# Performance work log

Measured on AMD Instinct MI355X. Metric: run time of the kernel, lower is better.

Reference implementation:

```python
import jax, jax.numpy as jnp
import numpy as np

EPS = 1e-5
N_HEADS = 8
NEG = -1e32


def _pos_emb(S, D):
    # CosinePositionalEmbedding: sin/cos fully overwrite the random init for even D
    pos = jnp.arange(S, dtype=jnp.float32)[:, None]
    div = jnp.exp(jnp.arange(0, D, 2, dtype=jnp.float32) * (-np.log(10000.0) / D))
    pe = jnp.zeros((S, D), dtype=jnp.float32)
    pe = pe.at[:, 0::2].set(jnp.sin(pos * div))
    pe = pe.at[:, 1::2].set(jnp.cos(pos * div))
    return pe


def _ln(x, g, b):
    mu = jnp.mean(x, axis=-1, keepdims=True)
    var = jnp.mean((x - mu) ** 2, axis=-1, keepdims=True)
    return (x - mu) / jnp.sqrt(var + EPS) * g + b


def setup_inputs() -> dict:
    key = jax.random.key(0)
    B, S, D, FF, L = 32, 512, 512, 2048, 4
    ks = jax.random.split(key, 8)
    w = 0.02
    return {
        "q_embed_data": jax.random.normal(ks[0], (B, S, D), jnp.float32),
        "qa_embed_data": jax.random.normal(ks[1], (B, S, D), jnp.float32),
        "boost_focus": jax.random.uniform(ks[2], (1,), jnp.float32),
        "Wk": w * jax.random.normal(ks[3], (L, D, D), jnp.float32),
        "bk": jnp.zeros((L, D), jnp.float32),
        "Wv": w * jax.random.normal(ks[4], (L, D, D), jnp.float32),
        "bv": jnp.zeros((L, D), jnp.float32),
        "Wo": w * jax.random.normal(ks[5], (L, D, D), jnp.float32),
        "bo": jnp.zeros((L, D), jnp.float32),
        "ln1_g": jnp.ones((L, D), jnp.float32),
        "ln1_b": jnp.zeros((L, D), jnp.float32),
        "W1": w * jax.random.normal(ks[6], (L, D, FF), jnp.float32),
        "b1": jnp.zeros((L, FF), jnp.float32),
        "W2": w * jax.random.normal(ks[7], (L, FF, D), jnp.float32),
        "b2": jnp.zeros((L, D), jnp.float32),
        "ln2_g": jnp.ones((L, D), jnp.float32),
        "ln2_b": jnp.zeros((L, D), jnp.float32),
    }


def reference(q_embed_data, qa_embed_data, boost_focus, Wk, bk, Wv, bv, Wo, bo,
              ln1_g, ln1_b, W1, b1, W2, b2, ln2_g, ln2_b):
    B, S, D = q_embed_data.shape
    L = Wk.shape[0]
    H = N_HEADS
    dk = D // H
    bf = boost_focus[0]
    pe = _pos_emb(S, D)
    x = q_embed_data + pe[None]          # query/key stream
    y = qa_embed_data + pe[None]         # value stream (fixed across blocks)
    # mask=0: triu(k=0)==0 -> only strictly past positions (j < i) allowed
    allowed = jnp.tril(jnp.ones((S, S), bool), k=-1)
    scale = 1.0 / np.sqrt(dk)
    for l in range(L):
        # kq_same=True: q and k both use k_linear on x -> identical projections
        qk = (x @ Wk[l] + bk[l]).reshape(B, S, H, dk).transpose(0, 2, 1, 3)
        v = (y @ Wv[l] + bv[l]).reshape(B, S, H, dk).transpose(0, 2, 1, 3)
        scores = jnp.einsum('bhid,bhjd->bhij', qk, qk) * scale * (1.0 + bf)
        scores = jnp.where(allowed, scores, NEG)
        probs = jax.nn.softmax(scores, axis=-1)
        probs = probs.at[:, :, 0, :].set(0.0)  # zero_pad: first query row zeroed
        attn = jnp.einsum('bhij,bhjd->bhid', probs, v)
        attn = attn.transpose(0, 2, 1, 3).reshape(B, S, D) @ Wo[l] + bo[l]
        x = _ln(x + attn, ln1_g[l], ln1_b[l])
        ff = jax.nn.relu(x @ W1[l] + b1[l]) @ W2[l] + b2[l]
        x = _ln(x + ff, ln2_g[l], ln2_b[l])
    return x
```

## Files before the change

### kernel.cpp

```cpp
#include <hip/hip_runtime.h>
#include <hip/hip_bf16.h>

typedef __bf16 bf16_t;
typedef __bf16 bf16x4 __attribute__((ext_vector_type(4)));
typedef __bf16 bf16x8 __attribute__((ext_vector_type(8)));
typedef float f32x4 __attribute__((ext_vector_type(4)));

union FragU { bf16x8 v; bf16x4 h[2]; };
union F4U { float4 v; float f[4]; };

constexpr int BB = 32, SS = 512, DD = 512, FFD = 2048, LL = 4, HH = 8;

__device__ __forceinline__ int permk(int k) {
  int g = (k >> 2) & 7;
  int pos = (g < 4) ? (g << 1) : (((g - 4) << 1) | 1);
  return (k & ~31) | (pos << 2) | (k & 3);
}

__device__ __forceinline__ void gload_lds16(const bf16_t* g, bf16_t* l) {
  __builtin_amdgcn_global_load_lds(
      (const __attribute__((address_space(1))) void*)g,
      (__attribute__((address_space(3))) void*)l, 16, 0, 0);
}

__global__ void pe_kernel(float* __restrict__ pe) {
  int idx = blockIdx.x * blockDim.x + threadIdx.x;
  if (idx >= SS * DD / 2) return;
  int p = idx % (DD / 2);
  int s = idx / (DD / 2);
  float div = expf((float)(2 * p) * (-9.210340371976184f / (float)DD));
  float a = (float)s * div;
  pe[s * DD + 2 * p]     = sinf(a);
  pe[s * DD + 2 * p + 1] = cosf(a);
}

__global__ __launch_bounds__(256) void tcast_kernel(const float* __restrict__ src,
                                                    bf16_t* __restrict__ dst,
                                                    int K, int N) {
  __shared__ float tile[32][33];
  size_t mat = (size_t)blockIdx.z * (size_t)K * (size_t)N;
  int k0 = blockIdx.y * 32, n0 = blockIdx.x * 32;
  int t = threadIdx.x;
  int r = t >> 3, c4 = (t & 7) * 4;
  const float4 v = *reinterpret_cast<const float4*>(&src[mat + (size_t)(k0 + r) * N + n0 + c4]);
  tile[r][c4 + 0] = v.x; tile[r][c4 + 1] = v.y; tile[r][c4 + 2] = v.z; tile[r][c4 + 3] = v.w;
  __syncthreads();
  bf16x4 o;
  o[0] = (bf16_t)tile[c4 + 0][r];
  o[1] = (bf16_t)tile[c4 + 1][r];
  o[2] = (bf16_t)tile[c4 + 2][r];
  o[3] = (bf16_t)tile[c4 + 3][r];
  *reinterpret_cast<bf16x4*>(&dst[mat + permk((n0 + r) * K + k0 + c4)]) = o;
}

__global__ void addpe_kernel(const float* __restrict__ q, const float* __restrict__ qa,
                             const float* __restrict__ pe,
                             float* __restrict__ x, bf16_t* __restrict__ xb,
                             bf16_t* __restrict__ yb) {
  int i = blockIdx.x * blockDim.x + threadIdx.x;
  int pei = i & (SS * DD / 4 - 1);
  float4 pv = reinterpret_cast<const float4*>(pe)[pei];
  float4 qv = reinterpret_cast<const float4*>(q)[i];
  float4 av = reinterpret_cast<const float4*>(qa)[i];
  float4 xv = make_float4(qv.x + pv.x, qv.y + pv.y, qv.z + pv.z, qv.w + pv.w);
  float4 yv = make_float4(av.x + pv.x, av.y + pv.y, av.z + pv.z, av.w + pv.w);
  reinterpret_cast<float4*>(x)[i] = xv;
  bf16x4 xo, yo;
  xo[0] = (bf16_t)xv.x; xo[1] = (bf16_t)xv.y; xo[2] = (bf16_t)xv.z; xo[3] = (bf16_t)xv.w;
  yo[0] = (bf16_t)yv.x; yo[1] = (bf16_t)yv.y; yo[2] = (bf16_t)yv.z; yo[3] = (bf16_t)yv.w;
  int kp = permk(4 * i);
  *reinterpret_cast<bf16x4*>(&xb[kp]) = xo;
  *reinterpret_cast<bf16x4*>(&yb[kp]) = yo;
}

template<bool OUT_BF16, bool RELU>
__global__ __launch_bounds__(256, 2) void gemm_kernel(const bf16_t* __restrict__ A,
                                                      const bf16_t* __restrict__ Bt,
                                                      const float* __restrict__ bias,
                                                      void* __restrict__ Cout,
                                                      int M, int N, int K, int nnt) {
  __shared__ bf16_t a_s[2][128 * 64];
  __shared__ bf16_t b_s[2][128 * 64];
  const int t = threadIdx.x;
  const int nwg = gridDim.x;
  const int bid = blockIdx.x;
  const int wg = (bid & 7) * (nwg >> 3) + (bid >> 3);
  const int m0 = (wg / nnt) * 128, n0 = (wg % nnt) * 128;
  const int l = t & 63, w = t >> 6, g = l >> 4, ln = l & 15;
  const int wm = (w >> 1) * 64, wn = (w & 1) * 64;
  const int tr = t >> 3;
  const int bsrc = ((t & 7) ^ (tr & 7)) * 8;
  const bf16_t* Asrc = A + (size_t)(m0 + tr) * K + bsrc;
  const bf16_t* Bsrc = Bt + (size_t)(n0 + tr) * K + bsrc;
  const size_t rstr = (size_t)32 * K;
  const int x0 = (g ^ (ln & 7)) * 8;
  const int x1 = ((4 + g) ^ (ln & 7)) * 8;
  f32x4 acc[4][4] = {};
  const int NT = K >> 6;
#pragma unroll
  for (int i = 0; i < 4; i++) gload_lds16(Asrc + i * rstr, &a_s[0][(i * 256 + t) * 8]);
#pragma unroll
  for (int i = 0; i < 4; i++) gload_lds16(Bsrc + i * rstr, &b_s[0][(i * 256 + t) * 8]);
  asm volatile("s_waitcnt vmcnt(0)" ::: "memory");
  __syncthreads();
  for (int tt = 0; tt < NT; tt++) {
    const int cur = tt & 1;
    if (tt + 1 < NT) {
      const int k1 = (tt + 1) << 6;
#pragma unroll
      for (int i = 0; i < 4; i++) gload_lds16(Asrc + k1 + i * rstr, &a_s[cur ^ 1][(i * 256 + t) * 8]);
#pragma unroll
      for (int i = 0; i < 4; i++) gload_lds16(Bsrc + k1 + i * rstr, &b_s[cur ^ 1][(i * 256 + t) * 8]);
    }
#pragma unroll
    for (int kc = 0; kc < 2; kc++) {
      const int xo = kc ? x1 : x0;
      FragU fa[4], fb[4];
#pragma unroll
      for (int mi = 0; mi < 4; mi++)
        fa[mi].v = *reinterpret_cast<const bf16x8*>(&a_s[cur][(wm + mi * 16 + ln) * 64 + xo]);
#pragma unroll
      for (int ni = 0; ni < 4; ni++)
        fb[ni].v = *reinterpret_cast<const bf16x8*>(&b_s[cur][(wn + ni * 16 + ln) * 64 + xo]);
      __builtin_amdgcn_s_setprio(1);
#pragma unroll
      for (int mi = 0; mi < 4; mi++)
#pragma unroll
        for (int ni = 0; ni < 4; ni++)
          acc[mi][ni] = __builtin_amdgcn_mfma_f32_16x16x32_bf16(fa[mi].v, fb[ni].v, acc[mi][ni], 0, 0, 0);
      __builtin_amdgcn_s_setprio(0);
    }
    asm volatile("s_waitcnt vmcnt(0)" ::: "memory");
    __syncthreads();
  }
#pragma unroll
  for (int ni = 0; ni < 4; ni++) {
    const int col = n0 + wn + ni * 16 + ln;
    const float bv = bias[col];
    const int colp = OUT_BF16 ? permk(col) : col;
#pragma unroll
    for (int mi = 0; mi < 4; mi++)
#pragma unroll
      for (int r = 0; r < 4; r++) {
        int row = m0 + wm + mi * 16 + g * 4 + r;
        float o = acc[mi][ni][r] + bv;
        if (RELU) o = fmaxf(o, 0.f);
        if (OUT_BF16)
          reinterpret_cast<bf16_t*>(Cout)[(size_t)row * N + colp] = (bf16_t)o;
        else
          reinterpret_cast<float*>(Cout)[(size_t)row * N + col] = o;
      }
  }
}

__global__ __launch_bounds__(256) void ln_kernel(const float* __restrict__ xin,
                                                 const float* __restrict__ addv,
                                                 const float* __restrict__ gamma,
                                                 const float* __restrict__ beta,
                                                 float* __restrict__ xout,
                                                 bf16_t* __restrict__ xbout) {
  int row = blockIdx.x * 4 + (threadIdx.x >> 6);
  int l = threadIdx.x & 63;
  const float* px = xin + (size_t)row * DD;
  const float* pa = addv + (size_t)row * DD;
  float vals[8];
  float s = 0.f;
#pragma unroll
  for (int i = 0; i < 2; i++) {
    float4 a = reinterpret_cast<const float4*>(px)[l * 2 + i];
    float4 b = reinterpret_cast<const float4*>(pa)[l * 2 + i];
    vals[i * 4 + 0] = a.x + b.x;
    vals[i * 4 + 1] = a.y + b.y;
    vals[i * 4 + 2] = a.z + b.z;
    vals[i * 4 + 3] = a.w + b.w;
  }
#pragma unroll
  for (int j = 0; j < 8; j++) s += vals[j];
#pragma unroll
  for (int off = 1; off < 64; off <<= 1) s += __shfl_xor(s, off, 64);
  float mean = s * (1.f / DD);
  float sq = 0.f;
#pragma unroll
  for (int j = 0; j < 8; j++) { float d = vals[j] - mean; sq += d * d; }
#pragma unroll
  for (int off = 1; off < 64; off <<= 1) sq += __shfl_xor(sq, off, 64);
  float rstd = rsqrtf(sq * (1.f / DD) + 1e-5f);
#pragma unroll
  for (int i = 0; i < 2; i++) {
    F4U o; bf16x4 ob;
#pragma unroll
    for (int j = 0; j < 4; j++) {
      int colj = l * 8 + i * 4 + j;
      float v = (vals[i * 4 + j] - mean) * rstd * gamma[colj] + beta[colj];
      o.f[j] = v;
      ob[j] = (bf16_t)v;
    }
    reinterpret_cast<float4*>(xout + (size_t)row * DD)[l * 2 + i] = o.v;
    *reinterpret_cast<bf16x4*>(&xbout[(size_t)row * DD + permk(l * 8 + i * 4)]) = ob;
  }
}

__global__ __launch_bounds__(256) void vtrans_kernel(const bf16_t* __restrict__ vbuf,
                                                     bf16_t* __restrict__ vtg) {
  __shared__ bf16_t t_s[64][72];
  const int jt = blockIdx.x, h = blockIdx.y, b = blockIdx.z;
  const int t = threadIdx.x;
#pragma unroll
  for (int i = 0; i < 2; i++) {
    int c = t + i * 256;
    int s = c >> 3, bb = c & 7;
    FragU vr;
    vr.v = *reinterpret_cast<const bf16x8*>(
        &vbuf[(size_t)(b * SS + jt * 64 + s) * DD + h * 64 + bb * 8]);
    int cc = (bb >> 2) * 32, p = (bb & 3) * 4;
    *reinterpret_cast<bf16x4*>(&t_s[s][cc + p]) = vr.h[0];
    *reinterpret_cast<bf16x4*>(&t_s[s][cc + 16 + p]) = vr.h[1];
  }
  __syncthreads();
#pragma unroll
  for (int i = 0; i < 2; i++) {
    int c = t + i * 256;
    int d = c >> 3, blkx = c & 7;
    int blk = blkx ^ (d & 7);
    int js = blk >> 2, g = blk & 3;
    FragU o;
#pragma unroll
    for (int e = 0; e < 4; e++) o.v[e] = t_s[js * 32 + g * 4 + e][d];
#pragma unroll
    for (int e = 0; e < 4; e++) o.v[e + 4] = t_s[js * 32 + 16 + g * 4 + e][d];
    *reinterpret_cast<bf16x8*>(
        &vtg[((size_t)((b * HH + h) * 64 + d)) * SS + jt * 64 + blkx * 8]) = o.v;
  }
}

__global__ __launch_bounds__(256) void attn_kernel(const bf16_t* __restrict__ qk,
                                                   const bf16_t* __restrict__ vtg,
                                                   bf16_t* __restrict__ outp,
                                                   const float* __restrict__ bfp) {
  __shared__ bf16_t k_s[64 * 64];
  __shared__ bf16_t v_t[64 * 64];
  const int bx = blockIdx.x, h = blockIdx.y, b = blockIdx.z;
  const int t = threadIdx.x, l = t & 63, w = t >> 6, g = l >> 4, ln = l & 15;
  const float sc = 0.125f * (1.f + bfp[0]);
  const size_t base = ((size_t)b * SS) * DD + h * 64;
  const bf16_t* vbase = vtg + ((size_t)((b * HH + h) * 64)) * SS;
  const int NQT = SS / 64;

  for (int pass = 0; pass < 2; pass++) {
    const int qt = pass ? (NQT - 1 - bx) : bx;
    const int i0 = qt * 64;
    FragU qB[2];
    {
      const bf16_t* qp = qk + base + (size_t)(i0 + w * 16 + ln) * DD;
      qB[0].v = *reinterpret_cast<const bf16x8*>(&qp[g * 8]);
      qB[1].v = *reinterpret_cast<const bf16x8*>(&qp[32 + g * 8]);
    }
    float m = -1e30f, lrow = 0.f;
    f32x4 acc[4] = {};
    const int iql = w * 16 + ln;

    for (int kt = 0; kt <= qt; kt++) {
      const int j0 = kt * 64;
      __syncthreads();
      {
        int c1 = t + 256;
        int jr0 = t >> 3, bb0 = t & 7;
        int jr1 = c1 >> 3, bb1 = c1 & 7;
        gload_lds16(qk + base + (size_t)(j0 + jr0) * DD + ((bb0 ^ (jr0 & 7)) * 8), &k_s[t * 8]);
        gload_lds16(qk + base + (size_t)(j0 + jr1) * DD + ((bb1 ^ (jr1 & 7)) * 8), &k_s[c1 * 8]);
        gload_lds16(vbase + (size_t)jr0 * SS + j0 + bb0 * 8, &v_t[t * 8]);
        gload_lds16(vbase + (size_t)jr1 * SS + j0 + bb1 * 8, &v_t[c1 * 8]);
      }
      asm volatile("s_waitcnt vmcnt(0)" ::: "memory");
      __syncthreads();
      f32x4 sfr[4] = {};
#pragma unroll
      for (int ks = 0; ks < 2; ks++)
#pragma unroll
        for (int nj = 0; nj < 4; nj++) {
          int jc = nj * 16 + ln;
          FragU ka;
          ka.v = *reinterpret_cast<const bf16x8*>(&k_s[jc * 64 + (((ks * 4 + g) ^ (jc & 7)) * 8)]);
          sfr[nj] = __builtin_amdgcn_mfma_f32_16x16x32_bf16(ka.v, qB[ks].v, sfr[nj], 0, 0, 0);
        }
      if (kt == qt) {
#pragma unroll
        for (int nj = 0; nj < 4; nj++)
#pragma unroll
          for (int r = 0; r < 4; r++)
            if (nj * 16 + g * 4 + r >= iql) sfr[nj][r] = -1e30f;
      }
      float pm = -1e30f;
#pragma unroll
      for (int nj = 0; nj < 4; nj++)
#pragma unroll
        for (int r = 0; r < 4; r++) pm = fmaxf(pm, sfr[nj][r]);
      pm = fmaxf(pm, __shfl_xor(pm, 16, 64));
      pm = fmaxf(pm, __shfl_xor(pm, 32, 64));
      float mnew = fmaxf(m, pm);
      float fac = __expf(sc * (m - mnew));
      m = mnew;
      float ps = 0.f;
#pragma unroll
      for (int nj = 0; nj < 4; nj++)
#pragma unroll
        for (int r = 0; r < 4; r++) {
          float p = __expf(sc * (sfr[nj][r] - m));
          sfr[nj][r] = p;
          ps += p;
        }
      ps += __shfl_xor(ps, 16, 64);
      ps += __shfl_xor(ps, 32, 64);
      lrow = lrow * fac + ps;
      float facr[4];
#pragma unroll
      for (int r = 0; r < 4; r++) facr[r] = __shfl(fac, g * 4 + r, 64);
#pragma unroll
      for (int nd = 0; nd < 4; nd++)
#pragma unroll
        for (int r = 0; r < 4; r++) acc[nd][r] *= facr[r];
      FragU pa[2];
#pragma unroll
      for (int js = 0; js < 2; js++)
#pragma unroll
        for (int kk = 0; kk < 4; kk++) {
          pa[js].v[kk]     = (bf16_t)sfr[js * 2][kk];
          pa[js].v[kk + 4] = (bf16_t)sfr[js * 2 + 1][kk];
        }
#pragma unroll
      for (int js = 0; js < 2; js++)
#pragma unroll
        for (int nd = 0; nd < 4; nd++) {
          int d = nd * 16 + ln;
          FragU vb;
          vb.v = *reinterpret_cast<const bf16x8*>(&v_t[d * 64 + (((js * 4 + g) ^ (d & 7)) * 8)]);
          acc[nd] = __builtin_amdgcn_mfma_f32_16x16x32_bf16(pa[js].v, vb.v, acc[nd], 0, 0, 0);
        }
    }
    float lr[4];
#pragma unroll
    for (int r = 0; r < 4; r++) lr[r] = __shfl(lrow, g * 4 + r, 64);
    const int orow0 = i0 + w * 16 + g * 4;
#pragma unroll
    for (int nd = 0; nd < 4; nd++) {
      const int colp = permk(nd * 16 + ln);
#pragma unroll
      for (int r = 0; r < 4; r++) {
        int grow = orow0 + r;
        float o = (grow > 0 && lr[r] > 0.f) ? acc[nd][r] / lr[r] : 0.f;
        outp[base + (size_t)grow * DD + colp] = (bf16_t)o;
      }
    }
  }
}

extern "C" void kernel_launch(void* const* d_in, const int* in_sizes, int n_in,
                              void* d_out, int out_size, void* d_ws, size_t ws_size,
                              hipStream_t stream) {
  const float* q_emb  = (const float*)d_in[0];
  const float* qa_emb = (const float*)d_in[1];
  const float* bfp    = (const float*)d_in[2];
  const float* Wk  = (const float*)d_in[3];
  const float* bk  = (const float*)d_in[4];
  const float* Wv  = (const float*)d_in[5];
  const float* bv  = (const float*)d_in[6];
  const float* Wo  = (const float*)d_in[7];
  const float* bo  = (const float*)d_in[8];
  const float* g1  = (const float*)d_in[9];
  const float* be1 = (const float*)d_in[10];
  const float* W1  = (const float*)d_in[11];
  const float* b1  = (const float*)d_in[12];
  const float* W2  = (const float*)d_in[13];
  const float* b2  = (const float*)d_in[14];
  const float* g2  = (const float*)d_in[15];
  const float* be2 = (const float*)d_in[16];
  float* out = (float*)d_out;
  (void)in_sizes; (void)n_in; (void)out_size; (void)ws_size;

  char* wsp = (char*)d_ws;
  size_t off = 0;
  auto alloc = [&](size_t bytes) -> void* {
    void* p = wsp + off;
    off += (bytes + 255) & ~(size_t)255;
    return p;
  };
  const size_t BSD = (size_t)BB * SS * DD;
  float*  pe   = (float*) alloc((size_t)SS * DD * 4);
  float*  x    = (float*) alloc(BSD * 4);
  float*  tmp  = (float*) alloc(BSD * 4);
  bf16_t* xb   = (bf16_t*)alloc(BSD * 2);
  bf16_t* yb   = (bf16_t*)alloc(BSD * 2);
  bf16_t* qkb  = (bf16_t*)alloc(BSD * 2);
  bf16_t* vbuf = (bf16_t*)alloc(BSD * 2);
  bf16_t* vtg  = (bf16_t*)alloc(BSD * 2);
  bf16_t* atb  = (bf16_t*)alloc(BSD * 2);
  bf16_t* h1   = (bf16_t*)alloc((size_t)BB * SS * FFD * 2);
  bf16_t* Wkb  = (bf16_t*)alloc((size_t)LL * DD * DD * 2);
  bf16_t* Wvb  = (bf16_t*)alloc((size_t)LL * DD * DD * 2);
  bf16_t* Wob  = (bf16_t*)alloc((size_t)LL * DD * DD * 2);
  bf16_t* W1b  = (bf16_t*)alloc((size_t)LL * DD * FFD * 2);
  bf16_t* W2b  = (bf16_t*)alloc((size_t)LL * FFD * DD * 2);

  pe_kernel<<<(SS * DD / 2 + 255) / 256, 256, 0, stream>>>(pe);
  tcast_kernel<<<dim3(DD / 32, DD / 32, LL), 256, 0, stream>>>(Wk, Wkb, DD, DD);
  tcast_kernel<<<dim3(DD / 32, DD / 32, LL), 256, 0, stream>>>(Wv, Wvb, DD, DD);
  tcast_kernel<<<dim3(DD / 32, DD / 32, LL), 256, 0, stream>>>(Wo, Wob, DD, DD);
  tcast_kernel<<<dim3(FFD / 32, DD / 32, LL), 256, 0, stream>>>(W1, W1b, DD, FFD);
  tcast_kernel<<<dim3(DD / 32, FFD / 32, LL), 256, 0, stream>>>(W2, W2b, FFD, DD);
  addpe_kernel<<<(int)(BSD / 4 / 256), 256, 0, stream>>>(q_emb, qa_emb, pe, x, xb, yb);

  const int M = BB * SS;
  const int nD = (M / 128) * (DD / 128);
  const int nF = (M / 128) * (FFD / 128);
  dim3 gA(SS / 128, HH, BB);
  dim3 gV(SS / 64, HH, BB);
  for (int layer = 0; layer < LL; layer++) {
    const bf16_t* Wkl = Wkb + (size_t)layer * DD * DD;
    const bf16_t* Wvl = Wvb + (size_t)layer * DD * DD;
    const bf16_t* Wol = Wob + (size_t)layer * DD * DD;
    const bf16_t* W1l = W1b + (size_t)layer * DD * FFD;
    const bf16_t* W2l = W2b + (size_t)layer * FFD * DD;
    gemm_kernel<true, false><<<nD, 256, 0, stream>>>(xb, Wkl, bk + layer * DD, qkb, M, DD, DD, DD / 128);
    gemm_kernel<true, false><<<nD, 256, 0, stream>>>(yb, Wvl, bv + layer * DD, vbuf, M, DD, DD, DD / 128);
    vtrans_kernel<<<gV, 256, 0, stream>>>(vbuf, vtg);
    attn_kernel<<<gA, 256, 0, stream>>>(qkb, vtg, atb, bfp);
    gemm_kernel<false, false><<<nD, 256, 0, stream>>>(atb, Wol, bo + layer * DD, tmp, M, DD, DD, DD / 128);
    ln_kernel<<<M / 4, 256, 0, stream>>>(x, tmp, g1 + layer * DD, be1 + layer * DD, x, xb);
    gemm_kernel<true, true><<<nF, 256, 0, stream>>>(xb, W1l, b1 + layer * FFD, h1, M, FFD, DD, FFD / 128);
    gemm_kernel<false, false><<<nD, 256, 0, stream>>>(h1, W2l, b2 + layer * DD, tmp, M, DD, FFD, DD / 128);
    float* xo = (layer == LL - 1) ? out : x;
    ln_kernel<<<M / 4, 256, 0, stream>>>(x, tmp, g2 + layer * DD, be2 + layer * DD, xo, xb);
  }
}
```

Before: 888.0 us.

## Replace GEMM with 8-wave 256-row tile kernel using ping-pong MFMA scheduling

Swaps the 128x128 tile, 4-wave GEMM for an 8-wave (512-thread) kernel with 256-row tiles, using 128 or 256 columns depending on the layer. Global-to-LDS loads now run two stages ahead, and LDS fragment reads are interleaved with MFMA clusters between barriers, in the style of the HipKittens 8-wave schedule. The larger tiles are meant to improve data reuse and keep the matrix units busy. In exchange, register pressure and barrier count go up, and the K/V/O GEMMs get fewer workgroups, which can hurt occupancy.

```diff
diff --git a/kernel.cpp b/kernel.cpp
--- a/kernel.cpp
+++ b/kernel.cpp
@@ -22,6 +22,12 @@
       (const __attribute__((address_space(1))) void*)g,
       (__attribute__((address_space(3))) void*)l, 16, 0, 0);
 }
+
+template<int N> __device__ __forceinline__ void vmwait() {
+  asm volatile("s_waitcnt vmcnt(%0)" :: "n"(N) : "memory");
+}
+
+#define MFMA_ACC(d, a, b) d = __builtin_amdgcn_mfma_f32_16x16x32_bf16((a).v, (b).v, d, 0, 0, 0)
 
 __global__ void pe_kernel(float* __restrict__ pe) {
   int idx = blockIdx.x * blockDim.x + threadIdx.x;
@@ -73,77 +79,177 @@
   *reinterpret_cast<bf16x4*>(&yb[kp]) = yo;
 }
 
-template<bool OUT_BF16, bool RELU>
-__global__ __launch_bounds__(256, 2) void gemm_kernel(const bf16_t* __restrict__ A,
-                                                      const bf16_t* __restrict__ Bt,
-                                                      const float* __restrict__ bias,
-                                                      void* __restrict__ Cout,
-                                                      int M, int N, int K, int nnt) {
-  __shared__ bf16_t a_s[2][128 * 64];
-  __shared__ bf16_t b_s[2][128 * 64];
+template<int BN, bool OUT_BF16, bool RELU>
+__global__ __launch_bounds__(512, 2) void gemm8_kernel(const bf16_t* __restrict__ A,
+                                                       const bf16_t* __restrict__ Bt,
+                                                       const float* __restrict__ bias,
+                                                       void* __restrict__ Cout,
+                                                       int N, int K, int nnt) {
+  constexpr int BM = 256, BK = 64;
+  constexpr int WN = BN / 4;
+  constexpr int NF = WN / 16;
+  constexpr int AL = 4, BL = BN / 64;
+  constexpr int LOADS = AL + BL;
+  __shared__ bf16_t a_s[2][BM * BK];
+  __shared__ bf16_t b_s[2][BN * BK];
   const int t = threadIdx.x;
-  const int nwg = gridDim.x;
-  const int bid = blockIdx.x;
+  const int bid = blockIdx.x, nwg = gridDim.x;
   const int wg = (bid & 7) * (nwg >> 3) + (bid >> 3);
-  const int m0 = (wg / nnt) * 128, n0 = (wg % nnt) * 128;
-  const int l = t & 63, w = t >> 6, g = l >> 4, ln = l & 15;
-  const int wm = (w >> 1) * 64, wn = (w & 1) * 64;
-  const int tr = t >> 3;
-  const int bsrc = ((t & 7) ^ (tr & 7)) * 8;
-  const bf16_t* Asrc = A + (size_t)(m0 + tr) * K + bsrc;
-  const bf16_t* Bsrc = Bt + (size_t)(n0 + tr) * K + bsrc;
-  const size_t rstr = (size_t)32 * K;
-  const int x0 = (g ^ (ln & 7)) * 8;
-  const int x1 = ((4 + g) ^ (ln & 7)) * 8;
-  f32x4 acc[4][4] = {};
+  const int m0 = (wg / nnt) * BM, n0 = (wg % nnt) * BN;
+  const int l = t & 63, w = t >> 6, g = l >> 4, ln = l & 15, lnx = l & 7;
+  const int wr = w >> 2, wc = w & 3;
+  const int tr8 = t >> 3;
+  const int bsrc = ((t & 7) ^ (tr8 & 7)) * 8;
+  const bf16_t* Asrc = A + (size_t)(m0 + tr8) * K + bsrc;
+  const bf16_t* Bsrc = Bt + (size_t)(n0 + tr8) * K + bsrc;
+  const size_t rstr = (size_t)64 * K;
+
+  auto STAGE = [&](int p, int kt) {
+    const int k0 = kt << 6;
+#pragma unroll
+    for (int i = 0; i < AL; i++) gload_lds16(Asrc + k0 + i * rstr, &a_s[p][(i * 512 + t) * 8]);
+#pragma unroll
+    for (int i = 0; i < BL; i++) gload_lds16(Bsrc + k0 + i * rstr, &b_s[p][(i * 512 + t) * 8]);
+  };
+  auto rdA = [&](int p, int mh, int mi, int kc) -> bf16x8 {
+    return *reinterpret_cast<const bf16x8*>(
+        &a_s[p][(wr * 128 + mh * 64 + mi * 16 + ln) * 64 + ((kc * 4 + g) ^ lnx) * 8]);
+  };
+  auto rdB = [&](int p, int nf, int kc) -> bf16x8 {
+    return *reinterpret_cast<const bf16x8*>(
+        &b_s[p][(wc * WN + nf * 16 + ln) * 64 + ((kc * 4 + g) ^ lnx) * 8]);
+  };
+
+  f32x4 acc[8][NF] = {};
   const int NT = K >> 6;
-#pragma unroll
-  for (int i = 0; i < 4; i++) gload_lds16(Asrc + i * rstr, &a_s[0][(i * 256 + t) * 8]);
-#pragma unroll
-  for (int i = 0; i < 4; i++) gload_lds16(Bsrc + i * rstr, &b_s[0][(i * 256 + t) * 8]);
-  asm volatile("s_waitcnt vmcnt(0)" ::: "memory");
+  STAGE(0, 0);
+  STAGE(1, 1);
+  vmwait<LOADS>();
   __syncthreads();
-  for (int tt = 0; tt < NT; tt++) {
-    const int cur = tt & 1;
-    if (tt + 1 < NT) {
-      const int k1 = (tt + 1) << 6;
-#pragma unroll
-      for (int i = 0; i < 4; i++) gload_lds16(Asrc + k1 + i * rstr, &a_s[cur ^ 1][(i * 256 + t) * 8]);
-#pragma unroll
-      for (int i = 0; i < 4; i++) gload_lds16(Bsrc + k1 + i * rstr, &b_s[cur ^ 1][(i * 256 + t) * 8]);
+
+  for (int T = 0; T < NT; T++) {
+    const int p = T & 1;
+    if constexpr (BN == 256) {
+      FragU fa[8], fbA[4], fbB[4];
+#pragma unroll
+      for (int kc = 0; kc < 2; kc++) {
+#pragma unroll
+        for (int mi = 0; mi < 4; mi++) fa[kc * 4 + mi].v = rdA(p, 0, mi, kc);
+#pragma unroll
+        for (int ni = 0; ni < 2; ni++) fbA[kc * 2 + ni].v = rdB(p, ni, kc);
+      }
+      __syncthreads();
+      __builtin_amdgcn_s_setprio(1);
+#pragma unroll
+      for (int kc = 0; kc < 2; kc++)
+#pragma unroll
+        for (int mi = 0; mi < 4; mi++)
+#pragma unroll
+          for (int ni = 0; ni < 2; ni++)
+            MFMA_ACC(acc[mi][ni], fa[kc * 4 + mi], fbA[kc * 2 + ni]);
+      __builtin_amdgcn_s_setprio(0);
+      __syncthreads();
+#pragma unroll
+      for (int kc = 0; kc < 2; kc++)
+#pragma unroll
+        for (int ni = 0; ni < 2; ni++) fbB[kc * 2 + ni].v = rdB(p, 2 + ni, kc);
+      __syncthreads();
+      __builtin_amdgcn_s_setprio(1);
+#pragma unroll
+      for (int kc = 0; kc < 2; kc++)
+#pragma unroll
+        for (int mi = 0; mi < 4; mi++)
+#pragma unroll
+          for (int ni = 0; ni < 2; ni++)
+            MFMA_ACC(acc[mi][2 + ni], fa[kc * 4 + mi], fbB[kc * 2 + ni]);
+      __builtin_amdgcn_s_setprio(0);
+      __syncthreads();
+#pragma unroll
+      for (int kc = 0; kc < 2; kc++)
+#pragma unroll
+        for (int mi = 0; mi < 4; mi++) fa[kc * 4 + mi].v = rdA(p, 1, mi, kc);
+      __syncthreads();
+      __builtin_amdgcn_s_setprio(1);
+#pragma unroll
+      for (int kc = 0; kc < 2; kc++)
+#pragma unroll
+        for (int mi = 0; mi < 4; mi++)
+#pragma unroll
+          for (int ni = 0; ni < 2; ni++)
+            MFMA_ACC(acc[4 + mi][2 + ni], fa[kc * 4 + mi], fbB[kc * 2 + ni]);
+      __builtin_amdgcn_s_setprio(0);
+      __syncthreads();
+      if (T + 2 < NT) STAGE(p, T + 2);
+      __syncthreads();
+      __builtin_amdgcn_s_setprio(1);
+#pragma unroll
+      for (int kc = 0; kc < 2; kc++)
+#pragma unroll
+        for (int mi = 0; mi < 4; mi++)
+#pragma unroll
+          for (int ni = 0; ni < 2; ni++)
+            MFMA_ACC(acc[4 + mi][ni], fa[kc * 4 + mi], fbA[kc * 2 + ni]);
+      __builtin_amdgcn_s_setprio(0);
+      if (T + 1 < NT) { if (T + 2 < NT) vmwait<LOADS>(); else vmwait<0>(); }
+      __syncthreads();
+    } else {
+      FragU fa0[8], fa1[8], fb[4];
+#pragma unroll
+      for (int kc = 0; kc < 2; kc++) {
+#pragma unroll
+        for (int mi = 0; mi < 4; mi++) fa0[kc * 4 + mi].v = rdA(p, 0, mi, kc);
+#pragma unroll
+        for (int ni = 0; ni < 2; ni++) fb[kc * 2 + ni].v = rdB(p, ni, kc);
+      }
+      __syncthreads();
+      __builtin_amdgcn_s_setprio(1);
+#pragma unroll
+      for (int mi = 0; mi < 4; mi++)
+#pragma unroll
+        for (int ni = 0; ni < 2; ni++)
+          MFMA_ACC(acc[mi][ni], fa0[mi], fb[ni]);
+      __builtin_amdgcn_s_setprio(0);
+      __syncthreads();
+#pragma unroll
+      for (int kc = 0; kc < 2; kc++)
+#pragma unroll
+        for (int mi = 0; mi < 4; mi++) fa1[kc * 4 + mi].v = rdA(p, 1, mi, kc);
+      __syncthreads();
+      __builtin_amdgcn_s_setprio(1);
+#pragma unroll
+      for (int mi = 0; mi < 4; mi++)
+#pragma unroll
+        for (int ni = 0; ni < 2; ni++)
+          MFMA_ACC(acc[mi][ni], fa0[4 + mi], fb[2 + ni]);
+      __builtin_amdgcn_s_setprio(0);
+      __syncthreads();
+      if (T + 2 < NT) STAGE(p, T + 2);
+      __syncthreads();
+      __builtin_amdgcn_s_setprio(1);
+#pragma unroll
+      for (int kc = 0; kc < 2; kc++)
+#pragma unroll
+        for (int mi = 0; mi < 4; mi++)
+#pragma unroll
+          for (int ni = 0; ni < 2; ni++)
+            MFMA_ACC(acc[4 + mi][ni], fa1[kc * 4 + mi], fb[kc * 2 + ni]);
+      __builtin_amdgcn_s_setprio(0);
+      if (T + 1 < NT) { if (T + 2 < NT) vmwait<LOADS>(); else vmwait<0>(); }
+      __syncthreads();
     }
-#pragma unroll
-    for (int kc = 0; kc < 2; kc++) {
-      const int xo = kc ? x1 : x0;
-      FragU fa[4], fb[4];
-#pragma unroll
-      for (int mi = 0; mi < 4; mi++)
-        fa[mi].v = *reinterpret_cast<const bf16x8*>(&a_s[cur][(wm + mi * 16 + ln) * 64 + xo]);
-#pragma unroll
-      for (int ni = 0; ni < 4; ni++)
-        fb[ni].v = *reinterpret_cast<const bf16x8*>(&b_s[cur][(wn + ni * 16 + ln) * 64 + xo]);
-      __builtin_amdgcn_s_setprio(1);
-#pragma unroll
-      for (int mi = 0; mi < 4; mi++)
-#pragma unroll
-        for (int ni = 0; ni < 4; ni++)
-          acc[mi][ni] = __builtin_amdgcn_mfma_f32_16x16x32_bf16(fa[mi].v, fb[ni].v, acc[mi][ni], 0, 0, 0);
-      __builtin_amdgcn_s_setprio(0);
-    }
-    asm volatile("s_waitcnt vmcnt(0)" ::: "memory");
-    __syncthreads();
-  }
-#pragma unroll
-  for (int ni = 0; ni < 4; ni++) {
-    const int col = n0 + wn + ni * 16 + ln;
+  }
+
+#pragma unroll
+  for (int nf = 0; nf < NF; nf++) {
+    const int col = n0 + wc * WN + nf * 16 + ln;
     const float bv = bias[col];
     const int colp = OUT_BF16 ? permk(col) : col;
 #pragma unroll
-    for (int mi = 0; mi < 4; mi++)
+    for (int mf = 0; mf < 8; mf++)
 #pragma unroll
       for (int r = 0; r < 4; r++) {
-        int row = m0 + wm + mi * 16 + g * 4 + r;
-        float o = acc[mi][ni][r] + bv;
+        int row = m0 + wr * 128 + mf * 16 + g * 4 + r;
+        float o = acc[mf][nf][r] + bv;
         if (RELU) o = fmaxf(o, 0.f);
         if (OUT_BF16)
           reinterpret_cast<bf16_t*>(Cout)[(size_t)row * N + colp] = (bf16_t)o;
@@ -410,8 +516,8 @@
   addpe_kernel<<<(int)(BSD / 4 / 256), 256, 0, stream>>>(q_emb, qa_emb, pe, x, xb, yb);
 
   const int M = BB * SS;
-  const int nD = (M / 128) * (DD / 128);
-  const int nF = (M / 128) * (FFD / 128);
+  const int nD8 = (M / 256) * (DD / 128);
+  const int nF8 = (M / 256) * (FFD / 256);
   dim3 gA(SS / 128, HH, BB);
   dim3 gV(SS / 64, HH, BB);
   for (int layer = 0; layer < LL; layer++) {
@@ -420,14 +526,14 @@
     const bf16_t* Wol = Wob + (size_t)layer * DD * DD;
     const bf16_t* W1l = W1b + (size_t)layer * DD * FFD;
     const bf16_t* W2l = W2b + (size_t)layer * FFD * DD;
-    gemm_kernel<true, false><<<nD, 256, 0, stream>>>(xb, Wkl, bk + layer * DD, qkb, M, DD, DD, DD / 128);
-    gemm_kernel<true, false><<<nD, 256, 0, stream>>>(yb, Wvl, bv + layer * DD, vbuf, M, DD, DD, DD / 128);
+    gemm8_kernel<128, true, false><<<nD8, 512, 0, stream>>>(xb, Wkl, bk + layer * DD, qkb, DD, DD, DD / 128);
+    gemm8_kernel<128, true, false><<<nD8, 512, 0, stream>>>(yb, Wvl, bv + layer * DD, vbuf, DD, DD, DD / 128);
     vtrans_kernel<<<gV, 256, 0, stream>>>(vbuf, vtg);
     attn_kernel<<<gA, 256, 0, stream>>>(qkb, vtg, atb, bfp);
-    gemm_kernel<false, false><<<nD, 256, 0, stream>>>(atb, Wol, bo + layer * DD, tmp, M, DD, DD, DD / 128);
+    gemm8_kernel<128, false, false><<<nD8, 512, 0, stream>>>(atb, Wol, bo + layer * DD, tmp, DD, DD, DD / 128);
     ln_kernel<<<M / 4, 256, 0, stream>>>(x, tmp, g1 + layer * DD, be1 + layer * DD, x, xb);
-    gemm_kernel<true, true><<<nF, 256, 0, stream>>>(xb, W1l, b1 + layer * FFD, h1, M, FFD, DD, FFD / 128);
-    gemm_kernel<false, false><<<nD, 256, 0, stream>>>(h1, W2l, b2 + layer * DD, tmp, M, DD, FFD, DD / 128);
+    gemm8_kernel<256, true, true><<<nF8, 512, 0, stream>>>(xb, W1l, b1 + layer * FFD, h1, FFD, DD, FFD / 256);
+    gemm8_kernel<128, false, false><<<nD8, 512, 0, stream>>>(h1, W2l, b2 + layer * DD, tmp, DD, FFD, DD / 128);
     float* xo = (layer == LL - 1) ? out : x;
     ln_kernel<<<M / 4, 256, 0, stream>>>(x, tmp, g2 + layer * DD, be2 + layer * DD, xo, xb);
   }
```

Result: slower. 1.085 ms (+22.2%).

## Fuse V transpose into V-projection GEMM epilogue and deepen GEMM prefetch

Applied to the files above, without the earlier changes.

The V-projection GEMM now writes its output directly in the transposed, swizzled per-head layout that the attention kernel reads. This removes the separate vtrans kernel and its intermediate buffer round-trip. The GEMM main loop also changes: it issues two stages ahead, waits with a partial vmcnt, and uses raw s_barrier with sched_barrier fences, so global loads overlap more with MFMA work. The transposed epilogue writes scattered 8-byte stores, which may coalesce less well than the old row-major stores.

```diff
diff --git a/kernel.cpp b/kernel.cpp
--- a/kernel.cpp
+++ b/kernel.cpp
@@ -21,6 +21,13 @@
   __builtin_amdgcn_global_load_lds(
       (const __attribute__((address_space(1))) void*)g,
       (__attribute__((address_space(3))) void*)l, 16, 0, 0);
+}
+
+template<int N> __device__ __forceinline__ void vmwait() {
+  asm volatile("s_waitcnt vmcnt(%0)" :: "n"(N) : "memory");
+}
+__device__ __forceinline__ void barrier_raw() {
+  asm volatile("s_barrier" ::: "memory");
 }
 
 __global__ void pe_kernel(float* __restrict__ pe) {
@@ -73,12 +80,12 @@
   *reinterpret_cast<bf16x4*>(&yb[kp]) = yo;
 }
 
-template<bool OUT_BF16, bool RELU>
+template<int OMODE, bool RELU>
 __global__ __launch_bounds__(256, 2) void gemm_kernel(const bf16_t* __restrict__ A,
                                                       const bf16_t* __restrict__ Bt,
                                                       const float* __restrict__ bias,
                                                       void* __restrict__ Cout,
-                                                      int M, int N, int K, int nnt) {
+                                                      int N, int K, int nnt) {
   __shared__ bf16_t a_s[2][128 * 64];
   __shared__ bf16_t b_s[2][128 * 64];
   const int t = threadIdx.x;
@@ -95,33 +102,34 @@
   const size_t rstr = (size_t)32 * K;
   const int x0 = (g ^ (ln & 7)) * 8;
   const int x1 = ((4 + g) ^ (ln & 7)) * 8;
+
+  auto STAGE = [&](int p, int T) {
+    const int k0 = T << 6;
+#pragma unroll
+    for (int i = 0; i < 4; i++) gload_lds16(Asrc + k0 + i * rstr, &a_s[p][(i * 256 + t) * 8]);
+#pragma unroll
+    for (int i = 0; i < 4; i++) gload_lds16(Bsrc + k0 + i * rstr, &b_s[p][(i * 256 + t) * 8]);
+  };
+
   f32x4 acc[4][4] = {};
   const int NT = K >> 6;
-#pragma unroll
-  for (int i = 0; i < 4; i++) gload_lds16(Asrc + i * rstr, &a_s[0][(i * 256 + t) * 8]);
-#pragma unroll
-  for (int i = 0; i < 4; i++) gload_lds16(Bsrc + i * rstr, &b_s[0][(i * 256 + t) * 8]);
-  asm volatile("s_waitcnt vmcnt(0)" ::: "memory");
-  __syncthreads();
-  for (int tt = 0; tt < NT; tt++) {
-    const int cur = tt & 1;
-    if (tt + 1 < NT) {
-      const int k1 = (tt + 1) << 6;
-#pragma unroll
-      for (int i = 0; i < 4; i++) gload_lds16(Asrc + k1 + i * rstr, &a_s[cur ^ 1][(i * 256 + t) * 8]);
-#pragma unroll
-      for (int i = 0; i < 4; i++) gload_lds16(Bsrc + k1 + i * rstr, &b_s[cur ^ 1][(i * 256 + t) * 8]);
-    }
+  STAGE(0, 0);
+  STAGE(1, 1);
+  for (int T = 0; T < NT; T++) {
+    const int p = T & 1;
+    if (T + 1 < NT) vmwait<8>(); else vmwait<0>();
+    barrier_raw();
+    __builtin_amdgcn_sched_barrier(0);
 #pragma unroll
     for (int kc = 0; kc < 2; kc++) {
       const int xo = kc ? x1 : x0;
       FragU fa[4], fb[4];
 #pragma unroll
       for (int mi = 0; mi < 4; mi++)
-        fa[mi].v = *reinterpret_cast<const bf16x8*>(&a_s[cur][(wm + mi * 16 + ln) * 64 + xo]);
+        fa[mi].v = *reinterpret_cast<const bf16x8*>(&a_s[p][(wm + mi * 16 + ln) * 64 + xo]);
 #pragma unroll
       for (int ni = 0; ni < 4; ni++)
-        fb[ni].v = *reinterpret_cast<const bf16x8*>(&b_s[cur][(wn + ni * 16 + ln) * 64 + xo]);
+        fb[ni].v = *reinterpret_cast<const bf16x8*>(&b_s[p][(wn + ni * 16 + ln) * 64 + xo]);
       __builtin_amdgcn_s_setprio(1);
 #pragma unroll
       for (int mi = 0; mi < 4; mi++)
@@ -130,26 +138,52 @@
           acc[mi][ni] = __builtin_amdgcn_mfma_f32_16x16x32_bf16(fa[mi].v, fb[ni].v, acc[mi][ni], 0, 0, 0);
       __builtin_amdgcn_s_setprio(0);
     }
-    asm volatile("s_waitcnt vmcnt(0)" ::: "memory");
-    __syncthreads();
-  }
-#pragma unroll
-  for (int ni = 0; ni < 4; ni++) {
-    const int col = n0 + wn + ni * 16 + ln;
-    const float bv = bias[col];
-    const int colp = OUT_BF16 ? permk(col) : col;
-#pragma unroll
-    for (int mi = 0; mi < 4; mi++)
-#pragma unroll
-      for (int r = 0; r < 4; r++) {
-        int row = m0 + wm + mi * 16 + g * 4 + r;
-        float o = acc[mi][ni][r] + bv;
-        if (RELU) o = fmaxf(o, 0.f);
-        if (OUT_BF16)
-          reinterpret_cast<bf16_t*>(Cout)[(size_t)row * N + colp] = (bf16_t)o;
-        else
-          reinterpret_cast<float*>(Cout)[(size_t)row * N + col] = o;
+    __builtin_amdgcn_sched_barrier(0);
+    barrier_raw();
+    if (T + 2 < NT) STAGE(p, T + 2);
+  }
+
+  if constexpr (OMODE == 2) {
+    const int brow = m0 >> 9;
+    const int s0b = (m0 & 511) + wm;
+    bf16_t* vout = reinterpret_cast<bf16_t*>(Cout);
+#pragma unroll
+    for (int ni = 0; ni < 4; ni++) {
+      const int d = n0 + wn + ni * 16 + ln;
+      const float bv = bias[d];
+      const int h = d >> 6, dd = d & 63;
+      bf16_t* vrow = vout + ((size_t)((brow * HH + h) * 64 + dd)) * SS;
+#pragma unroll
+      for (int mi = 0; mi < 4; mi++) {
+        const int s0 = s0b + mi * 16 + g * 4;
+        const int jt = s0 >> 6, jj = s0 & 63;
+        const int js = jj >> 5, half = (jj >> 4) & 1;
+        const int blkx = (js * 4 + g) ^ (dd & 7);
+        bf16x4 o;
+#pragma unroll
+        for (int r = 0; r < 4; r++) o[r] = (bf16_t)(acc[mi][ni][r] + bv);
+        *reinterpret_cast<bf16x4*>(&vrow[jt * 64 + blkx * 8 + half * 4]) = o;
       }
+    }
+  } else {
+#pragma unroll
+    for (int ni = 0; ni < 4; ni++) {
+      const int col = n0 + wn + ni * 16 + ln;
+      const float bv = bias[col];
+      const int colp = (OMODE == 1) ? permk(col) : col;
+#pragma unroll
+      for (int mi = 0; mi < 4; mi++)
+#pragma unroll
+        for (int r = 0; r < 4; r++) {
+          int row = m0 + wm + mi * 16 + g * 4 + r;
+          float o = acc[mi][ni][r] + bv;
+          if (RELU) o = fmaxf(o, 0.f);
+          if (OMODE == 1)
+            reinterpret_cast<bf16_t*>(Cout)[(size_t)row * N + colp] = (bf16_t)o;
+          else
+            reinterpret_cast<float*>(Cout)[(size_t)row * N + col] = o;
+        }
+    }
   }
 }
 
@@ -197,39 +231,6 @@
     }
     reinterpret_cast<float4*>(xout + (size_t)row * DD)[l * 2 + i] = o.v;
     *reinterpret_cast<bf16x4*>(&xbout[(size_t)row * DD + permk(l * 8 + i * 4)]) = ob;
-  }
-}
-
-__global__ __launch_bounds__(256) void vtrans_kernel(const bf16_t* __restrict__ vbuf,
-                                                     bf16_t* __restrict__ vtg) {
-  __shared__ bf16_t t_s[64][72];
-  const int jt = blockIdx.x, h = blockIdx.y, b = blockIdx.z;
-  const int t = threadIdx.x;
-#pragma unroll
-  for (int i = 0; i < 2; i++) {
-    int c = t + i * 256;
-    int s = c >> 3, bb = c & 7;
-    FragU vr;
-    vr.v = *reinterpret_cast<const bf16x8*>(
-        &vbuf[(size_t)(b * SS + jt * 64 + s) * DD + h * 64 + bb * 8]);
-    int cc = (bb >> 2) * 32, p = (bb & 3) * 4;
-    *reinterpret_cast<bf16x4*>(&t_s[s][cc + p]) = vr.h[0];
-    *reinterpret_cast<bf16x4*>(&t_s[s][cc + 16 + p]) = vr.h[1];
-  }
-  __syncthreads();
-#pragma unroll
-  for (int i = 0; i < 2; i++) {
-    int c = t + i * 256;
-    int d = c >> 3, blkx = c & 7;
-    int blk = blkx ^ (d & 7);
-    int js = blk >> 2, g = blk & 3;
-    FragU o;
-#pragma unroll
-    for (int e = 0; e < 4; e++) o.v[e] = t_s[js * 32 + g * 4 + e][d];
-#pragma unroll
-    for (int e = 0; e < 4; e++) o.v[e + 4] = t_s[js * 32 + 16 + g * 4 + e][d];
-    *reinterpret_cast<bf16x8*>(
-        &vtg[((size_t)((b * HH + h) * 64 + d)) * SS + jt * 64 + blkx * 8]) = o.v;
   }
 }
 
@@ -391,7 +392,6 @@
   bf16_t* xb   = (bf16_t*)alloc(BSD * 2);
   bf16_t* yb   = (bf16_t*)alloc(BSD * 2);
   bf16_t* qkb  = (bf16_t*)alloc(BSD * 2);
-  bf16_t* vbuf = (bf16_t*)alloc(BSD * 2);
   bf16_t* vtg  = (bf16_t*)alloc(BSD * 2);
   bf16_t* atb  = (bf16_t*)alloc(BSD * 2);
   bf16_t* h1   = (bf16_t*)alloc((size_t)BB * SS * FFD * 2);
@@ -413,21 +413,19 @@
   const int nD = (M / 128) * (DD / 128);
   const int nF = (M / 128) * (FFD / 128);
   dim3 gA(SS / 128, HH, BB);
-  dim3 gV(SS / 64, HH, BB);
   for (int layer = 0; layer < LL; layer++) {
     const bf16_t* Wkl = Wkb + (size_t)layer * DD * DD;
     const bf16_t* Wvl = Wvb + (size_t)layer * DD * DD;
     const bf16_t* Wol = Wob + (size_t)layer * DD * DD;
     const bf16_t* W1l = W1b + (size_t)layer * DD * FFD;
     const bf16_t* W2l = W2b + (size_t)layer * FFD * DD;
-    gemm_kernel<true, false><<<nD, 256, 0, stream>>>(xb, Wkl, bk + layer * DD, qkb, M, DD, DD, DD / 128);
-    gemm_kernel<true, false><<<nD, 256, 0, stream>>>(yb, Wvl, bv + layer * DD, vbuf, M, DD, DD, DD / 128);
-    vtrans_kernel<<<gV, 256, 0, stream>>>(vbuf, vtg);
+    gemm_kernel<1, false><<<nD, 256, 0, stream>>>(xb, Wkl, bk + layer * DD, qkb, DD, DD, DD / 128);
+    gemm_kernel<2, false><<<nD, 256, 0, stream>>>(yb, Wvl, bv + layer * DD, vtg, DD, DD, DD / 128);
     attn_kernel<<<gA, 256, 0, stream>>>(qkb, vtg, atb, bfp);
-    gemm_kernel<false, false><<<nD, 256, 0, stream>>>(atb, Wol, bo + layer * DD, tmp, M, DD, DD, DD / 128);
+    gemm_kernel<0, false><<<nD, 256, 0, stream>>>(atb, Wol, bo + layer * DD, tmp, DD, DD, DD / 128);
     ln_kernel<<<M / 4, 256, 0, stream>>>(x, tmp, g1 + layer * DD, be1 + layer * DD, x, xb);
-    gemm_kernel<true, true><<<nF, 256, 0, stream>>>(xb, W1l, b1 + layer * FFD, h1, M, FFD, DD, FFD / 128);
-    gemm_kernel<false, false><<<nD, 256, 0, stream>>>(h1, W2l, b2 + layer * DD, tmp, M, DD, FFD, DD / 128);
+    gemm_kernel<1, true><<<nF, 256, 0, stream>>>(xb, W1l, b1 + layer * FFD, h1, FFD, DD, FFD / 128);
+    gemm_kernel<0, false><<<nD, 256, 0, stream>>>(h1, W2l, b2 + layer * DD, tmp, DD, FFD, DD / 128);
     float* xo = (layer == LL - 1) ? out : x;
     ln_kernel<<<M / 4, 256, 0, stream>>>(x, tmp, g2 + layer * DD, be2 + layer * DD, xo, xb);
   }
```

New measurement: 828.5 us. 6.7% less time.
